# Kernel tuning notes

Measured on AMD Instinct MI355X. Metric: run time of the kernel, lower is better.

## Reference

```python
import jax, jax.numpy as jnp
import numpy as np

D_MODEL = 1024
D_STATE = 64
D_CONV = 4
EXPAND = 2
HEADDIM = 128
NGROUPS = 1
D_INNER = EXPAND * D_MODEL                      # 2048
NHEADS = D_INNER // HEADDIM                     # 16
CONV_DIM = D_INNER + 2 * NGROUPS * D_STATE      # 2176
D_IN_PROJ = 2 * D_INNER + 2 * NGROUPS * D_STATE + NHEADS  # 4240
CHUNK = 64
B, L = 4, 2048


def segsum(x):
    # x: (..., l) -> (..., l, l); entry [i, j] = sum_{k=j+1..i} x_k (lower-tri, -inf above)
    l = x.shape[-1]
    cs = jnp.cumsum(x, -1)
    d = cs[..., :, None] - cs[..., None, :]
    mask = jnp.tril(jnp.ones((l, l), bool))
    return jnp.where(mask, d, -jnp.inf)


def setup_inputs() -> dict:
    key = jax.random.key(0)
    ks = jax.random.split(key, 8)
    x = jax.random.normal(ks[0], (B, L), jnp.float32)
    w_embed = jax.random.normal(ks[1], (D_MODEL,), jnp.float32)       # Linear(1, d_model) weight
    ln_g = jnp.ones((D_MODEL,), jnp.float32)
    ln_b = jnp.zeros((D_MODEL,), jnp.float32)
    W_in = jax.random.normal(ks[2], (D_IN_PROJ, D_MODEL), jnp.float32) * 0.02
    conv_w = jax.random.normal(ks[3], (CONV_DIM, D_CONV), jnp.float32) * 0.1
    conv_b = jnp.zeros((CONV_DIM,), jnp.float32)
    dt0 = jnp.exp(jax.random.uniform(ks[4], (NHEADS,), jnp.float32) * (np.log(0.1) - np.log(0.001)) + np.log(0.001))
    dt_bias = jnp.log(jnp.expm1(dt0))  # inverse softplus (mamba2 init)
    A_log = jnp.log(jax.random.uniform(ks[5], (NHEADS,), jnp.float32, minval=1.0, maxval=16.0))
    D = jnp.ones((NHEADS,), jnp.float32)
    rms_w = jnp.ones((D_INNER,), jnp.float32)
    W_out = jax.random.normal(ks[6], (D_MODEL, D_INNER), jnp.float32) * 0.02
    return {"x": x, "w_embed": w_embed, "ln_g": ln_g, "ln_b": ln_b, "W_in": W_in,
            "conv_w": conv_w, "conv_b": conv_b, "dt_bias": dt_bias, "A_log": A_log,
            "D": D, "rms_w": rms_w, "W_out": W_out}


def reference(x, w_embed, ln_g, ln_b, W_in, conv_w, conv_b, dt_bias, A_log, D, rms_w, W_out):
    # in_proj: Linear(1, d_model, bias=False)
    h = x[..., None] * w_embed                     # (B, L, d_model)
    # LayerNorm
    mu = jnp.mean(h, -1, keepdims=True)
    var = jnp.mean((h - mu) ** 2, -1, keepdims=True)
    h = (h - mu) * jax.lax.rsqrt(var + 1e-5) * ln_g + ln_b
    # ---- Mamba2 block ----
    zxbcdt = h @ W_in.T                            # (B, L, D_IN_PROJ)
    z, xBC, dt = jnp.split(zxbcdt, [D_INNER, D_INNER + CONV_DIM], axis=-1)
    dt = jax.nn.softplus(dt + dt_bias)             # (B, L, H)
    # causal depthwise conv1d + silu
    xp = jnp.pad(xBC, ((0, 0), (D_CONV - 1, 0), (0, 0)))
    conv = conv_b + sum(xp[:, k:k + L, :] * conv_w[:, k] for k in range(D_CONV))
    xBC = jax.nn.silu(conv)
    xs, Bm, Cm = jnp.split(xBC, [D_INNER, D_INNER + NGROUPS * D_STATE], axis=-1)
    X = xs.reshape(B, L, NHEADS, HEADDIM)
    rep = NHEADS // NGROUPS
    Bh = jnp.repeat(Bm.reshape(B, L, NGROUPS, D_STATE), rep, axis=2)   # (B,L,H,N)
    Ch = jnp.repeat(Cm.reshape(B, L, NGROUPS, D_STATE), rep, axis=2)
    A = -jnp.exp(A_log)                            # (H,)
    dA = dt * A                                    # (B, L, H)
    Xd = X * dt[..., None]                         # (B, L, H, P)
    # chunked SSD scan (math-equivalent to the selective-scan recurrence)
    nc = L // CHUNK
    Xc = Xd.reshape(B, nc, CHUNK, NHEADS, HEADDIM)
    Bc = Bh.reshape(B, nc, CHUNK, NHEADS, D_STATE)
    Cc = Ch.reshape(B, nc, CHUNK, NHEADS, D_STATE)
    Ac = dA.reshape(B, nc, CHUNK, NHEADS).transpose(0, 3, 1, 2)        # (B,H,c,l)
    Acs = jnp.cumsum(Ac, -1)
    Lmat = jnp.exp(segsum(Ac))                                          # (B,H,c,l,l)
    Y_diag = jnp.einsum('bclhn,bcshn,bhcls,bcshp->bclhp', Cc, Bc, Lmat, Xc)
    decay_states = jnp.exp(Acs[..., -1:] - Acs)
    states = jnp.einsum('bclhn,bhcl,bclhp->bchpn', Bc, decay_states, Xc)
    states = jnp.concatenate([jnp.zeros_like(states[:, :1]), states], axis=1)
    decay_chunk = jnp.exp(segsum(jnp.pad(Acs[..., -1], ((0, 0), (0, 0), (1, 0)))))
    prev_states = jnp.einsum('bhzc,bchpn->bzhpn', decay_chunk, states)[:, :-1]
    Y_off = jnp.einsum('bclhn,bchpn,bhcl->bclhp', Cc, prev_states, jnp.exp(Acs))
    Y = (Y_diag + Y_off).reshape(B, L, NHEADS, HEADDIM) + X * D[None, None, :, None]
    y = Y.reshape(B, L, D_INNER)
    # gated RMSNorm then out_proj
    y = y * jax.nn.silu(z)
    y = y * jax.lax.rsqrt(jnp.mean(y * y, -1, keepdims=True) + 1e-5) * rms_w
    return y @ W_out.T
```

## Files before the change

kernel.cpp:

```cpp
#include <hip/hip_runtime.h>

#define DEV __device__ __forceinline__

typedef __bf16 bf16x8 __attribute__((ext_vector_type(8)));
typedef float f32x4 __attribute__((ext_vector_type(4)));

#define BB 4
#define LL 2048
#define DMODEL 1024
#define DINNER 2048
#define NHEADS 16
#define HEADDIM 128
#define DSTATE 64
#define CONVDIM 2176
#define DINPROJ 4240
#define NCHUNK 32
#define ROWS (BB*LL)

#define OF_A    ((size_t)0)
#define OF_ST   ((size_t)32768)
#define OF_P    ((size_t)65536)
#define OF_Q    ((size_t)98304)
#define OF_WO   ((size_t)131072)
#define OF_Y    ((size_t)50331648)
#define OF_YBF  ((size_t)100663296)
#define OF_SP   ((size_t)150994944)
#define OF_ACS  ((size_t)190840832)
#define OF_ECS  ((size_t)191365120)

DEV void gload_lds16(const void* g, void* l) {
  __builtin_amdgcn_global_load_lds((const __attribute__((address_space(1))) void*)g,
                                   (__attribute__((address_space(3))) void*)l, 16, 0, 0);
}

DEV char* swaddr(char* base, int r, int c) {
  return base + r * 128 + (((c) * 2) ^ (((r) & 7) << 4));
}

DEV float convsilu(int ch, const float* __restrict__ conv_w, const float* __restrict__ conv_b,
                   const float* __restrict__ p, const float* __restrict__ q,
                   const float av[4], const float mk[4]) {
  f32x4 w4 = *(const f32x4*)(conv_w + ch * 4);
  float sa = av[0] * w4[0] + av[1] * w4[1] + av[2] * w4[2] + av[3] * w4[3];
  float sm = mk[0] * w4[0] + mk[1] * w4[1] + mk[2] * w4[2] + mk[3] * w4[3];
  float val = conv_b[ch] + q[DINNER + ch] * sm + p[DINNER + ch] * sa;
  return val / (1.f + __expf(-val));
}

__global__ __launch_bounds__(256) void stats_kernel(
    const float* __restrict__ w, float* __restrict__ st)
{
  int t = threadIdx.x;
  float s = 0.f, s2 = 0.f;
  #pragma unroll
  for (int j = 0; j < 4; j++) { float v = w[t + 256 * j]; s += v; s2 += v * v; }
  #pragma unroll
  for (int m = 32; m; m >>= 1) { s += __shfl_xor(s, m); s2 += __shfl_xor(s2, m); }
  __shared__ float rs[4], rs2[4];
  if ((t & 63) == 0) { rs[t >> 6] = s; rs2[t >> 6] = s2; }
  __syncthreads();
  if (t == 0) {
    float S = rs[0] + rs[1] + rs[2] + rs[3];
    float S2 = rs2[0] + rs2[1] + rs2[2] + rs2[3];
    float mu = S * (1.f / DMODEL);
    st[0] = mu;
    st[1] = S2 * (1.f / DMODEL) - mu * mu;
  }
}

__global__ __launch_bounds__(256) void prep_a_kernel(
    const float* __restrict__ x, const float* __restrict__ st, float* __restrict__ a)
{
  int r = blockIdx.x * 256 + threadIdx.x;
  float varw = st[1];
  float xv = x[r];
  a[r] = xv * rsqrtf(xv * xv * varw + 1e-5f);
}

__global__ __launch_bounds__(256) void gemv_kernel(
    const float* __restrict__ w, const float* __restrict__ g,
    const float* __restrict__ beta, const float* __restrict__ st,
    const float* __restrict__ W, float* __restrict__ p, float* __restrict__ q)
{
  int t = threadIdx.x;
  int j = blockIdx.x * 16 + (t >> 4);
  int l16 = t & 15;
  float wbar = st[0];
  const float* Wr = W + (size_t)j * DMODEL;
  float ap = 0.f, aq = 0.f;
  #pragma unroll 4
  for (int jj = 0; jj < 64; jj++) {
    int i = jj * 16 + l16;
    float Wv = Wr[i];
    ap += (w[i] - wbar) * g[i] * Wv;
    aq += beta[i] * Wv;
  }
  #pragma unroll
  for (int m = 8; m; m >>= 1) { ap += __shfl_xor(ap, m, 16); aq += __shfl_xor(aq, m, 16); }
  if (l16 == 0) { p[j] = ap; q[j] = aq; }
}

__global__ __launch_bounds__(256) void convert_wo_kernel(
    const float* __restrict__ Wo, __bf16* __restrict__ Wob)
{
  const int NO = DMODEL * DINNER;
  for (int i = blockIdx.x * 256 + threadIdx.x; i < NO; i += gridDim.x * 256)
    Wob[i] = (__bf16)Wo[i];
}

__global__ __launch_bounds__(256) void ssd_chunk_kernel(
    const float* __restrict__ a, const float* __restrict__ p,
    const float* __restrict__ q, const float* __restrict__ conv_w,
    const float* __restrict__ conv_b, const float* __restrict__ dt_bias,
    const float* __restrict__ A_log,
    __bf16* __restrict__ Y, __bf16* __restrict__ S,
    float* __restrict__ acs, float* __restrict__ ecs)
{
  __shared__ __align__(16) char sm[49664];
  char* smC  = sm;
  char* smB  = sm + 8192;
  char* smBd = sm + 16384;
  char* smG  = sm + 24576;
  char* smX  = sm + 32768;
  float* sAcs = (float*)(sm + 49152);
  float* sDec = (float*)(sm + 49408);

  int bx = blockIdx.x;
  int c = bx & 31, h = (bx >> 5) & 15, b = bx >> 9;
  int t = threadIdx.x;
  int lane = t & 63, w = t >> 6;
  int row0 = b * LL + c * 64;

  float av[4], mk[4];
  {
    int lg = c * 64 + lane;
    #pragma unroll
    for (int k = 0; k < 4; k++) {
      int li = lg + k - 3;
      bool v = li >= 0;
      av[k] = v ? a[b * LL + li] : 0.f;
      mk[k] = v ? 1.f : 0.f;
    }
  }

  float vx = av[3] * p[DINNER + CONVDIM + h] + q[DINNER + CONVDIM + h] + dt_bias[h];
  float dtv = vx > 15.f ? vx : log1pf(__expf(vx));

  float bv[16];
  #pragma unroll
  for (int k = 0; k < 2; k++) {
    int c8 = w * 16 + 8 * k;
    bf16x8 vb, vc;
    #pragma unroll
    for (int j = 0; j < 8; j++) {
      int n = c8 + j;
      float bb = convsilu(2048 + n, conv_w, conv_b, p, q, av, mk);
      float cc = convsilu(2112 + n, conv_w, conv_b, p, q, av, mk);
      bv[8 * k + j] = bb;
      vb[j] = (__bf16)bb;
      vc[j] = (__bf16)cc;
    }
    *(bf16x8*)swaddr(smB, lane, c8) = vb;
    *(bf16x8*)swaddr(smC, lane, c8) = vc;
  }
  #pragma unroll
  for (int k = 0; k < 4; k++) {
    int p0 = w * 8 + 32 * k;
    #pragma unroll
    for (int j = 0; j < 8; j++) {
      float xv2 = convsilu(h * HEADDIM + p0 + j, conv_w, conv_b, p, q, av, mk);
      *(__bf16*)swaddr(smX, p0 + j, lane) = (__bf16)(xv2 * dtv);
    }
  }

  if (t < 64) {
    float Ah = -__expf(A_log[h]);
    float cs = dtv * Ah;
    #pragma unroll
    for (int off = 1; off < 64; off <<= 1) {
      float o = __shfl_up(cs, off);
      if (lane >= off) cs += o;
    }
    float cend = __shfl(cs, 63);
    sAcs[lane] = cs;
    sDec[lane] = __expf(cend - cs);
    acs[(((size_t)b * NHEADS + h) * NCHUNK + c) * 64 + lane] = cs;
    if (lane == 63) ecs[((size_t)b * NHEADS + h) * NCHUNK + c] = __expf(cend);
  }
  __syncthreads();

  float decv = sDec[lane];
  #pragma unroll
  for (int k = 0; k < 2; k++) {
    int c8 = w * 16 + 8 * k;
    #pragma unroll
    for (int j = 0; j < 8; j++)
      *(__bf16*)swaddr(smBd, c8 + j, lane) = (__bf16)(bv[8 * k + j] * decv);
  }

  int lr = lane & 15, kb = (lane >> 4) * 8;
  int rl = 16 * w + (lane >> 4) * 4;

  {
    bf16x8 af[2];
    #pragma unroll
    for (int ks = 0; ks < 2; ks++)
      af[ks] = *(const bf16x8*)swaddr(smC, 16 * w + lr, ks * 32 + kb);
    f32x4 g[4] = {};
    #pragma unroll
    for (int nt = 0; nt < 4; nt++)
      #pragma unroll
      for (int ks = 0; ks < 2; ks++) {
        bf16x8 bm = *(const bf16x8*)swaddr(smB, 16 * nt + lr, ks * 32 + kb);
        g[nt] = __builtin_amdgcn_mfma_f32_16x16x32_bf16(af[ks], bm, g[nt], 0, 0, 0);
      }
    #pragma unroll
    for (int nt = 0; nt < 4; nt++)
      #pragma unroll
      for (int qq = 0; qq < 4; qq++) {
        int gl = rl + qq, gs = 16 * nt + lr;
        float val = (gl >= gs) ? g[nt][qq] * __expf(sAcs[gl] - sAcs[gs]) : 0.f;
        *(__bf16*)swaddr(smG, gl, gs) = (__bf16)val;
      }
  }
  __syncthreads();

  {
    bf16x8 af[2];
    #pragma unroll
    for (int ks = 0; ks < 2; ks++)
      af[ks] = *(const bf16x8*)swaddr(smG, 16 * w + lr, ks * 32 + kb);
    f32x4 y[8] = {};
    #pragma unroll
    for (int nt = 0; nt < 8; nt++)
      #pragma unroll
      for (int ks = 0; ks < 2; ks++) {
        bf16x8 bm = *(const bf16x8*)swaddr(smX, 16 * nt + lr, ks * 32 + kb);
        y[nt] = __builtin_amdgcn_mfma_f32_16x16x32_bf16(af[ks], bm, y[nt], 0, 0, 0);
      }
    #pragma unroll
    for (int nt = 0; nt < 8; nt++)
      #pragma unroll
      for (int qq = 0; qq < 4; qq++)
        Y[(size_t)(row0 + rl + qq) * DINNER + h * HEADDIM + 16 * nt + lr] = (__bf16)y[nt][qq];
  }

  {
    bf16x8 bfs[4][2];
    #pragma unroll
    for (int nt = 0; nt < 4; nt++)
      #pragma unroll
      for (int ks = 0; ks < 2; ks++)
        bfs[nt][ks] = *(const bf16x8*)swaddr(smBd, 16 * nt + lr, ks * 32 + kb);
    f32x4 s4[2][4] = {};
    #pragma unroll
    for (int mi = 0; mi < 2; mi++) {
      bf16x8 af[2];
      #pragma unroll
      for (int ks = 0; ks < 2; ks++)
        af[ks] = *(const bf16x8*)swaddr(smX, 32 * w + 16 * mi + lr, ks * 32 + kb);
      #pragma unroll
      for (int nt = 0; nt < 4; nt++)
        #pragma unroll
        for (int ks = 0; ks < 2; ks++)
          s4[mi][nt] = __builtin_amdgcn_mfma_f32_16x16x32_bf16(af[ks], bfs[nt][ks], s4[mi][nt], 0, 0, 0);
    }
    __bf16* Sp = S + (((size_t)b * NCHUNK + c) * NHEADS + h) * (HEADDIM * DSTATE);
    #pragma unroll
    for (int mi = 0; mi < 2; mi++)
      #pragma unroll
      for (int nt = 0; nt < 4; nt++)
        #pragma unroll
        for (int qq = 0; qq < 4; qq++) {
          int pp = 32 * w + 16 * mi + (lane >> 4) * 4 + qq;
          Sp[pp * DSTATE + 16 * nt + lr] = (__bf16)s4[mi][nt][qq];
        }
  }
}

__global__ __launch_bounds__(256) void scan_kernel(
    __bf16* SP, const float* __restrict__ ecs)
{
  int t = blockIdx.x * 256 + threadIdx.x;
  int n = t & 63, p = (t >> 6) & 127, h = (t >> 13) & 15, b = t >> 17;
  float P = 0.f;
  for (int c = 0; c < NCHUNK; c++) {
    size_t idx = (((size_t)b * NCHUNK + c) * NHEADS + h) * (HEADDIM * DSTATE) + (size_t)p * DSTATE + n;
    float s = (float)SP[idx];
    SP[idx] = (__bf16)P;
    float e = ecs[((size_t)b * NHEADS + h) * NCHUNK + c];
    P = e * P + s;
  }
}

__global__ __launch_bounds__(256) void ssd_off_kernel(
    const float* __restrict__ a, const float* __restrict__ p,
    const float* __restrict__ q, const float* __restrict__ conv_w,
    const float* __restrict__ conv_b, const __bf16* __restrict__ P,
    const float* __restrict__ acs, const float* __restrict__ Dp,
    __bf16* __restrict__ Y)
{
  __shared__ __align__(16) char sm[25408];
  char* smC = sm;
  char* smP = sm + 8192;
  float* eA = (float*)(sm + 24576);
  float* sA = (float*)(sm + 24832);
  int bx = blockIdx.x;
  int c = bx & 31, h = (bx >> 5) & 15, b = bx >> 9;
  int t = threadIdx.x;
  int lane = t & 63, w = t >> 6;
  int row0 = b * LL + c * 64;

  {
    float av[4], mk[4];
    int lg = c * 64 + lane;
    #pragma unroll
    for (int k = 0; k < 4; k++) {
      int li = lg + k - 3;
      bool v = li >= 0;
      av[k] = v ? a[b * LL + li] : 0.f;
      mk[k] = v ? 1.f : 0.f;
    }
    #pragma unroll
    for (int k = 0; k < 2; k++) {
      int c8 = w * 16 + 8 * k;
      bf16x8 vc;
      #pragma unroll
      for (int j = 0; j < 8; j++)
        vc[j] = (__bf16)convsilu(2112 + c8 + j, conv_w, conv_b, p, q, av, mk);
      *(bf16x8*)swaddr(smC, lane, c8) = vc;
    }
  }
  if (t < 67) {
    int li = c * 64 + t - 3;
    sA[t] = (li >= 0) ? a[b * LL + li] : 0.f;
  }
  const __bf16* Pp = P + (((size_t)b * NCHUNK + c) * NHEADS + h) * (HEADDIM * DSTATE);
  #pragma unroll
  for (int k = 0; k < 4; k++) {
    int qg = t + 256 * k;
    int pr = qg >> 3, c8 = (qg & 7) * 8;
    bf16x8 v = *(const bf16x8*)(Pp + pr * DSTATE + c8);
    *(bf16x8*)swaddr(smP, pr, c8) = v;
  }
  if (t < 64) eA[t] = __expf(acs[(((size_t)b * NHEADS + h) * NCHUNK + c) * 64 + t]);
  __syncthreads();

  int lr = lane & 15, kb = (lane >> 4) * 8;
  bf16x8 af[2];
  #pragma unroll
  for (int ks = 0; ks < 2; ks++)
    af[ks] = *(const bf16x8*)swaddr(smC, 16 * w + lr, ks * 32 + kb);
  f32x4 y[8] = {};
  #pragma unroll
  for (int nt = 0; nt < 8; nt++)
    #pragma unroll
    for (int ks = 0; ks < 2; ks++) {
      bf16x8 bm = *(const bf16x8*)swaddr(smP, 16 * nt + lr, ks * 32 + kb);
      y[nt] = __builtin_amdgcn_mfma_f32_16x16x32_bf16(af[ks], bm, y[nt], 0, 0, 0);
    }
  float Dh = Dp[h];
  int rl = 16 * w + (lane >> 4) * 4;
  #pragma unroll
  for (int nt = 0; nt < 8; nt++) {
    int ch = h * HEADDIM + 16 * nt + lr;
    f32x4 w4 = *(const f32x4*)(conv_w + ch * 4);
    float cb = conv_b[ch], px = p[DINNER + ch], qx = q[DINNER + ch];
    #pragma unroll
    for (int qq = 0; qq < 4; qq++) {
      int l = rl + qq;
      float sa = sA[l] * w4[0] + sA[l + 1] * w4[1] + sA[l + 2] * w4[2] + sA[l + 3] * w4[3];
      float smv;
      if (c > 0) smv = w4[0] + w4[1] + w4[2] + w4[3];
      else {
        smv = w4[3];
        #pragma unroll
        for (int k = 0; k < 3; k++) if (l + k >= 3) smv += w4[k];
      }
      float val = cb + qx * smv + px * sa;
      float xsv = val / (1.f + __expf(-val));
      size_t yi = (size_t)(row0 + l) * DINNER + ch;
      Y[yi] = (__bf16)((float)Y[yi] + eA[l] * y[nt][qq] + Dh * xsv);
    }
  }
}

__global__ __launch_bounds__(256) void gate_norm_kernel(
    const __bf16* __restrict__ Y, const float* __restrict__ a,
    const float* __restrict__ p, const float* __restrict__ q,
    const float* __restrict__ rms_w, __bf16* __restrict__ ybf)
{
  int row = blockIdx.x, t = threadIdx.x;
  float ar = a[row];
  float v[8]; float ss = 0.f;
  #pragma unroll
  for (int j = 0; j < 8; j++) {
    int i = t + j * 256;
    float zv = ar * p[i] + q[i];
    float yv = (float)Y[(size_t)row * DINNER + i];
    float g = yv * (zv / (1.f + __expf(-zv)));
    v[j] = g; ss += g * g;
  }
  #pragma unroll
  for (int m = 32; m; m >>= 1) ss += __shfl_xor(ss, m);
  __shared__ float red[4];
  if ((t & 63) == 0) red[t >> 6] = ss;
  __syncthreads();
  float tot = red[0] + red[1] + red[2] + red[3];
  float r = rsqrtf(tot * (1.f / DINNER) + 1e-5f);
  #pragma unroll
  for (int j = 0; j < 8; j++) {
    int i = t + j * 256;
    ybf[(size_t)row * DINNER + i] = (__bf16)(v[j] * r * rms_w[i]);
  }
}

__global__ __launch_bounds__(512, 2) void gemm_op_kernel(
    const __bf16* __restrict__ A, const __bf16* __restrict__ Bt,
    float* __restrict__ C, int K, int N)
{
  extern __shared__ char sm[];
  const int t = threadIdx.x;
  const int lane = t & 63, w = t >> 6;
  const int wr = w >> 1, wc = w & 1;

  int nbn = gridDim.x;
  int nwg = nbn * gridDim.y;
  int lid = blockIdx.y * nbn + blockIdx.x;
  int wg = (lid & 7) * (nwg >> 3) + (lid >> 3);
  int m0 = (wg / nbn) * 256, n0 = (wg % nbn) * 128;

  int r0, c0, r1, c1;
  {
    int y0 = t * 16, pg0 = y0 >> 7;
    int in0 = (y0 & 127) ^ ((pg0 & 7) << 4);
    r0 = pg0 * 2 + (in0 >> 6); c0 = in0 & 63;
    int y1 = 8192 + t * 16, pg1 = y1 >> 7;
    int in1 = (y1 & 127) ^ ((pg1 & 7) << 4);
    r1 = pg1 * 2 + (in1 >> 6); c1 = in1 & 63;
  }
  const char* pA0 = (const char*)A + (size_t)(m0 + r0) * (2 * K) + c0;
  const char* pA1 = (const char*)A + (size_t)(m0 + r1) * (2 * K) + c1;
  const char* pB0 = (const char*)Bt + (size_t)(n0 + r0) * (2 * K) + c0;

  const int lr = lane & 15, kg = lane >> 4;
  int rA = wr * 64 + lr, pgA = rA >> 1;
  const int offA = pgA * 128 + ((((rA & 1) << 6) | (kg << 4)) ^ ((pgA & 7) << 4));
  int rB = wc * 64 + lr, pgB = rB >> 1;
  const int offB = pgB * 128 + ((((rB & 1) << 6) | (kg << 4)) ^ ((pgB & 7) << 4));

  f32x4 acc[4][4] = {};
  const int KT = K >> 5;

  #define STG(slot) do { \
    char* la_ = sm + (slot) * 16384; \
    char* lb_ = sm + 65536 + (slot) * 8192; \
    gload_lds16(pA0, la_ + t * 16); \
    gload_lds16(pA1, la_ + 8192 + t * 16); \
    gload_lds16(pB0, lb_ + t * 16); \
    pA0 += 64; pA1 += 64; pB0 += 64; \
  } while (0)

  STG(0); STG(1); STG(2);
  asm volatile("s_waitcnt vmcnt(6)" ::: "memory");
  __builtin_amdgcn_sched_barrier(0);
  __builtin_amdgcn_s_barrier();

  for (int kt = 0; kt < KT; ++kt) {
    int s = kt & 3;
    if (kt + 3 < KT) STG((kt + 3) & 3);
    const char* sa = sm + s * 16384;
    const char* sb = sm + 65536 + s * 8192;
    bf16x8 af[4], bfr[4];
    #pragma unroll
    for (int m = 0; m < 4; m++) af[m] = *(const bf16x8*)(sa + offA + m * 1024);
    #pragma unroll
    for (int n = 0; n < 4; n++) bfr[n] = *(const bf16x8*)(sb + offB + n * 1024);
    __builtin_amdgcn_s_setprio(1);
    #pragma unroll
    for (int m = 0; m < 4; m++)
      #pragma unroll
      for (int n = 0; n < 4; n++)
        acc[m][n] = __builtin_amdgcn_mfma_f32_16x16x32_bf16(af[m], bfr[n], acc[m][n], 0, 0, 0);
    __builtin_amdgcn_s_setprio(0);
    if (kt + 3 < KT)      { asm volatile("s_waitcnt vmcnt(6)" ::: "memory"); }
    else if (kt + 2 < KT) { asm volatile("s_waitcnt vmcnt(3)" ::: "memory"); }
    else if (kt + 1 < KT) { asm volatile("s_waitcnt vmcnt(0)" ::: "memory"); }
    __builtin_amdgcn_sched_barrier(0);
    __builtin_amdgcn_s_barrier();
  }
  #undef STG

  #pragma unroll
  for (int m = 0; m < 4; m++)
    #pragma unroll
    for (int n = 0; n < 4; n++)
      #pragma unroll
      for (int qq = 0; qq < 4; qq++) {
        int row = m0 + wr * 64 + m * 16 + kg * 4 + qq;
        int col = n0 + wc * 64 + n * 16 + lr;
        C[(size_t)row * N + col] = acc[m][n][qq];
      }
}

extern "C" void kernel_launch(void* const* d_in, const int* in_sizes, int n_in,
                              void* d_out, int out_size, void* d_ws, size_t ws_size,
                              hipStream_t stream) {
  const float* x       = (const float*)d_in[0];
  const float* w_embed = (const float*)d_in[1];
  const float* ln_g    = (const float*)d_in[2];
  const float* ln_b    = (const float*)d_in[3];
  const float* W_in    = (const float*)d_in[4];
  const float* conv_w  = (const float*)d_in[5];
  const float* conv_b  = (const float*)d_in[6];
  const float* dt_bias = (const float*)d_in[7];
  const float* A_log   = (const float*)d_in[8];
  const float* Dp      = (const float*)d_in[9];
  const float* rms_w   = (const float*)d_in[10];
  const float* W_out   = (const float*)d_in[11];
  char* ws = (char*)d_ws;
  float*  aR   = (float*)(ws + OF_A);
  float*  st   = (float*)(ws + OF_ST);
  float*  pV   = (float*)(ws + OF_P);
  float*  qV   = (float*)(ws + OF_Q);
  __bf16* Wob  = (__bf16*)(ws + OF_WO);
  __bf16* Ybf  = (__bf16*)(ws + OF_Y);
  __bf16* ybf  = (__bf16*)(ws + OF_YBF);
  __bf16* SP   = (__bf16*)(ws + OF_SP);
  float*  acs  = (float*)(ws + OF_ACS);
  float*  ecs  = (float*)(ws + OF_ECS);
  float*  out  = (float*)d_out;

  hipFuncSetAttribute((const void*)gemm_op_kernel,
                      hipFuncAttributeMaxDynamicSharedMemorySize, 98304);

  stats_kernel<<<1, 256, 0, stream>>>(w_embed, st);
  prep_a_kernel<<<ROWS / 256, 256, 0, stream>>>(x, st, aR);
  gemv_kernel<<<DINPROJ / 16, 256, 0, stream>>>(w_embed, ln_g, ln_b, st, W_in, pV, qV);
  convert_wo_kernel<<<1024, 256, 0, stream>>>(W_out, Wob);
  ssd_chunk_kernel<<<BB * NHEADS * NCHUNK, 256, 0, stream>>>(
      aR, pV, qV, conv_w, conv_b, dt_bias, A_log, Ybf, SP, acs, ecs);
  scan_kernel<<<(BB * NHEADS * HEADDIM * DSTATE) / 256, 256, 0, stream>>>(SP, ecs);
  ssd_off_kernel<<<BB * NHEADS * NCHUNK, 256, 0, stream>>>(
      aR, pV, qV, conv_w, conv_b, SP, acs, Dp, Ybf);
  gate_norm_kernel<<<ROWS, 256, 0, stream>>>(Ybf, aR, pV, qV, rms_w, ybf);
  gemm_op_kernel<<<dim3(8, 32), 512, 98304, stream>>>(ybf, Wob, out, DINNER, DMODEL);
}
```

Baseline: 255.3 us.

## Precompute conv-SiLU B/C once, vectorize scan and gemv, use fast reciprocal silu

Adds a bc_kernel that computes the conv+SiLU B and C projections once per row into a bf16 buffer. Previously every head block recomputed them redundantly in both ssd_chunk and ssd_off. The scan kernel now has each thread handle 8 state elements with 16-byte loads and stores, and the gemv uses float4 loads. SiLU now uses a hardware reciprocal instead of a division. The costs are an extra launch, a 2 MB intermediate buffer, and small precision differences.

```diff
diff --git a/kernel.cpp b/kernel.cpp
--- a/kernel.cpp
+++ b/kernel.cpp
@@ -22,6 +22,7 @@
 #define OF_P    ((size_t)65536)
 #define OF_Q    ((size_t)98304)
 #define OF_WO   ((size_t)131072)
+#define OF_BC   ((size_t)4325376)
 #define OF_Y    ((size_t)50331648)
 #define OF_YBF  ((size_t)100663296)
 #define OF_SP   ((size_t)150994944)
@@ -35,6 +36,10 @@
 
 DEV char* swaddr(char* base, int r, int c) {
   return base + r * 128 + (((c) * 2) ^ (((r) & 7) << 4));
+}
+
+DEV float fsilu(float v) {
+  return v * __builtin_amdgcn_rcpf(1.f + __expf(-v));
 }
 
 DEV float convsilu(int ch, const float* __restrict__ conv_w, const float* __restrict__ conv_b,
@@ -44,7 +49,7 @@
   float sa = av[0] * w4[0] + av[1] * w4[1] + av[2] * w4[2] + av[3] * w4[3];
   float sm = mk[0] * w4[0] + mk[1] * w4[1] + mk[2] * w4[2] + mk[3] * w4[3];
   float val = conv_b[ch] + q[DINNER + ch] * sm + p[DINNER + ch] * sa;
-  return val / (1.f + __expf(-val));
+  return fsilu(val);
 }
 
 __global__ __launch_bounds__(256) void stats_kernel(
@@ -89,11 +94,17 @@
   const float* Wr = W + (size_t)j * DMODEL;
   float ap = 0.f, aq = 0.f;
   #pragma unroll 4
-  for (int jj = 0; jj < 64; jj++) {
-    int i = jj * 16 + l16;
-    float Wv = Wr[i];
-    ap += (w[i] - wbar) * g[i] * Wv;
-    aq += beta[i] * Wv;
+  for (int jj = 0; jj < 16; jj++) {
+    int i = jj * 64 + l16 * 4;
+    f32x4 Wv = *(const f32x4*)(Wr + i);
+    f32x4 wv = *(const f32x4*)(w + i);
+    f32x4 gv = *(const f32x4*)(g + i);
+    f32x4 bv = *(const f32x4*)(beta + i);
+    #pragma unroll
+    for (int e = 0; e < 4; e++) {
+      ap += (wv[e] - wbar) * gv[e] * Wv[e];
+      aq += bv[e] * Wv[e];
+    }
   }
   #pragma unroll
   for (int m = 8; m; m >>= 1) { ap += __shfl_xor(ap, m, 16); aq += __shfl_xor(aq, m, 16); }
@@ -106,13 +117,37 @@
   const int NO = DMODEL * DINNER;
   for (int i = blockIdx.x * 256 + threadIdx.x; i < NO; i += gridDim.x * 256)
     Wob[i] = (__bf16)Wo[i];
+}
+
+__global__ __launch_bounds__(256) void bc_kernel(
+    const float* __restrict__ a, const float* __restrict__ p,
+    const float* __restrict__ q, const float* __restrict__ conv_w,
+    const float* __restrict__ conv_b, __bf16* __restrict__ BC)
+{
+  int g = blockIdx.x * 256 + threadIdx.x;
+  if (g >= ROWS * 16) return;
+  int cg = g & 15, row = g >> 4;
+  int l = row & (LL - 1);
+  float av[4], mk[4];
+  #pragma unroll
+  for (int k = 0; k < 4; k++) {
+    int li = l + k - 3;
+    bool v = li >= 0;
+    av[k] = v ? a[row + k - 3] : 0.f;
+    mk[k] = v ? 1.f : 0.f;
+  }
+  bf16x8 o;
+  #pragma unroll
+  for (int j = 0; j < 8; j++)
+    o[j] = (__bf16)convsilu(DINNER + cg * 8 + j, conv_w, conv_b, p, q, av, mk);
+  *(bf16x8*)(BC + (size_t)row * 128 + cg * 8) = o;
 }
 
 __global__ __launch_bounds__(256) void ssd_chunk_kernel(
     const float* __restrict__ a, const float* __restrict__ p,
     const float* __restrict__ q, const float* __restrict__ conv_w,
     const float* __restrict__ conv_b, const float* __restrict__ dt_bias,
-    const float* __restrict__ A_log,
+    const float* __restrict__ A_log, const __bf16* __restrict__ BC,
     __bf16* __restrict__ Y, __bf16* __restrict__ S,
     float* __restrict__ acs, float* __restrict__ ecs)
 {
@@ -146,20 +181,15 @@
   float vx = av[3] * p[DINNER + CONVDIM + h] + q[DINNER + CONVDIM + h] + dt_bias[h];
   float dtv = vx > 15.f ? vx : log1pf(__expf(vx));
 
+  const __bf16* bcr = BC + (size_t)(row0 + lane) * 128;
   float bv[16];
   #pragma unroll
   for (int k = 0; k < 2; k++) {
     int c8 = w * 16 + 8 * k;
-    bf16x8 vb, vc;
-    #pragma unroll
-    for (int j = 0; j < 8; j++) {
-      int n = c8 + j;
-      float bb = convsilu(2048 + n, conv_w, conv_b, p, q, av, mk);
-      float cc = convsilu(2112 + n, conv_w, conv_b, p, q, av, mk);
-      bv[8 * k + j] = bb;
-      vb[j] = (__bf16)bb;
-      vc[j] = (__bf16)cc;
-    }
+    bf16x8 vb = *(const bf16x8*)(bcr + c8);
+    bf16x8 vc = *(const bf16x8*)(bcr + 64 + c8);
+    #pragma unroll
+    for (int j = 0; j < 8; j++) bv[8 * k + j] = (float)vb[j];
     *(bf16x8*)swaddr(smB, lane, c8) = vb;
     *(bf16x8*)swaddr(smC, lane, c8) = vc;
   }
@@ -282,21 +312,30 @@
     __bf16* SP, const float* __restrict__ ecs)
 {
   int t = blockIdx.x * 256 + threadIdx.x;
-  int n = t & 63, p = (t >> 6) & 127, h = (t >> 13) & 15, b = t >> 17;
-  float P = 0.f;
+  int n8 = (t & 7) * 8, p = (t >> 3) & 127, h = (t >> 10) & 15, b = t >> 14;
+  const float* ep = ecs + ((size_t)b * NHEADS + h) * NCHUNK;
+  float P[8] = {};
+  size_t base = (((size_t)b * NCHUNK * NHEADS + h) * (HEADDIM * DSTATE)) + (size_t)p * DSTATE + n8;
+  const size_t cstride = (size_t)NHEADS * HEADDIM * DSTATE;
   for (int c = 0; c < NCHUNK; c++) {
-    size_t idx = (((size_t)b * NCHUNK + c) * NHEADS + h) * (HEADDIM * DSTATE) + (size_t)p * DSTATE + n;
-    float s = (float)SP[idx];
-    SP[idx] = (__bf16)P;
-    float e = ecs[((size_t)b * NHEADS + h) * NCHUNK + c];
-    P = e * P + s;
+    __bf16* ptr = SP + base + (size_t)c * cstride;
+    bf16x8 s = *(const bf16x8*)ptr;
+    bf16x8 o;
+    float e = ep[c];
+    #pragma unroll
+    for (int j = 0; j < 8; j++) {
+      o[j] = (__bf16)P[j];
+      P[j] = e * P[j] + (float)s[j];
+    }
+    *(bf16x8*)ptr = o;
   }
 }
 
 __global__ __launch_bounds__(256) void ssd_off_kernel(
     const float* __restrict__ a, const float* __restrict__ p,
     const float* __restrict__ q, const float* __restrict__ conv_w,
-    const float* __restrict__ conv_b, const __bf16* __restrict__ P,
+    const float* __restrict__ conv_b, const __bf16* __restrict__ BC,
+    const __bf16* __restrict__ P,
     const float* __restrict__ acs, const float* __restrict__ Dp,
     __bf16* __restrict__ Y)
 {
@@ -312,22 +351,11 @@
   int row0 = b * LL + c * 64;
 
   {
-    float av[4], mk[4];
-    int lg = c * 64 + lane;
-    #pragma unroll
-    for (int k = 0; k < 4; k++) {
-      int li = lg + k - 3;
-      bool v = li >= 0;
-      av[k] = v ? a[b * LL + li] : 0.f;
-      mk[k] = v ? 1.f : 0.f;
-    }
+    const __bf16* bcr = BC + (size_t)(row0 + lane) * 128;
     #pragma unroll
     for (int k = 0; k < 2; k++) {
       int c8 = w * 16 + 8 * k;
-      bf16x8 vc;
-      #pragma unroll
-      for (int j = 0; j < 8; j++)
-        vc[j] = (__bf16)convsilu(2112 + c8 + j, conv_w, conv_b, p, q, av, mk);
+      bf16x8 vc = *(const bf16x8*)(bcr + 64 + c8);
       *(bf16x8*)swaddr(smC, lane, c8) = vc;
     }
   }
@@ -377,8 +405,7 @@
         #pragma unroll
         for (int k = 0; k < 3; k++) if (l + k >= 3) smv += w4[k];
       }
-      float val = cb + qx * smv + px * sa;
-      float xsv = val / (1.f + __expf(-val));
+      float xsv = fsilu(cb + qx * smv + px * sa);
       size_t yi = (size_t)(row0 + l) * DINNER + ch;
       Y[yi] = (__bf16)((float)Y[yi] + eA[l] * y[nt][qq] + Dh * xsv);
     }
@@ -398,7 +425,7 @@
     int i = t + j * 256;
     float zv = ar * p[i] + q[i];
     float yv = (float)Y[(size_t)row * DINNER + i];
-    float g = yv * (zv / (1.f + __expf(-zv)));
+    float g = yv * fsilu(zv);
     v[j] = g; ss += g * g;
   }
   #pragma unroll
@@ -524,6 +551,7 @@
   float*  pV   = (float*)(ws + OF_P);
   float*  qV   = (float*)(ws + OF_Q);
   __bf16* Wob  = (__bf16*)(ws + OF_WO);
+  __bf16* BCb  = (__bf16*)(ws + OF_BC);
   __bf16* Ybf  = (__bf16*)(ws + OF_Y);
   __bf16* ybf  = (__bf16*)(ws + OF_YBF);
   __bf16* SP   = (__bf16*)(ws + OF_SP);
@@ -538,11 +566,12 @@
   prep_a_kernel<<<ROWS / 256, 256, 0, stream>>>(x, st, aR);
   gemv_kernel<<<DINPROJ / 16, 256, 0, stream>>>(w_embed, ln_g, ln_b, st, W_in, pV, qV);
   convert_wo_kernel<<<1024, 256, 0, stream>>>(W_out, Wob);
+  bc_kernel<<<(ROWS * 16) / 256, 256, 0, stream>>>(aR, pV, qV, conv_w, conv_b, BCb);
   ssd_chunk_kernel<<<BB * NHEADS * NCHUNK, 256, 0, stream>>>(
-      aR, pV, qV, conv_w, conv_b, dt_bias, A_log, Ybf, SP, acs, ecs);
-  scan_kernel<<<(BB * NHEADS * HEADDIM * DSTATE) / 256, 256, 0, stream>>>(SP, ecs);
+      aR, pV, qV, conv_w, conv_b, dt_bias, A_log, BCb, Ybf, SP, acs, ecs);
+  scan_kernel<<<(BB * NHEADS * HEADDIM * DSTATE / 8) / 256, 256, 0, stream>>>(SP, ecs);
   ssd_off_kernel<<<BB * NHEADS * NCHUNK, 256, 0, stream>>>(
-      aR, pV, qV, conv_w, conv_b, SP, acs, Dp, Ybf);
+      aR, pV, qV, conv_w, conv_b, BCb, SP, acs, Dp, Ybf);
   gate_norm_kernel<<<ROWS, 256, 0, stream>>>(Ybf, aR, pV, qV, rms_w, ybf);
   gemm_op_kernel<<<dim3(8, 32), 512, 98304, stream>>>(ybf, Wob, out, DINNER, DMODEL);
 }
```

Result: faster. 239.0 us (-6.4%).
